# Kernel optimization log

Hardware: AMD Instinct MI355X
Metric: run time of the kernel (lower is better)

Reference implementation:

```python
import jax, jax.numpy as jnp
import numpy as np

N = 50000      # nodes
E = 1600000    # edges
R = 12         # relations (num_unique_edge_attrs)
F_IN = 64      # num_node_features
H = 128        # hidden_channels
C = 10         # num_classes
G = 256        # graphs in batch
EPS = 1e-5     # BatchNorm eps


def setup_inputs() -> dict:
    key = jax.random.key(0)
    ks = jax.random.split(key, 10)
    s = 0.05
    return {
        "x": jax.random.normal(ks[0], (N, F_IN), jnp.float32),
        "Wrel1": jax.random.normal(ks[1], (R, F_IN, H), jnp.float32) * s,
        "root1": jax.random.normal(ks[2], (F_IN, H), jnp.float32) * s,
        "bias1": jnp.zeros((H,), jnp.float32),
        "gamma1": jnp.ones((H,), jnp.float32),
        "beta1": jnp.zeros((H,), jnp.float32),
        "Wrel2": jax.random.normal(ks[3], (R, H, H), jnp.float32) * s,
        "root2": jax.random.normal(ks[4], (H, H), jnp.float32) * s,
        "bias2": jnp.zeros((H,), jnp.float32),
        "gamma2": jnp.ones((H,), jnp.float32),
        "beta2": jnp.zeros((H,), jnp.float32),
        "Wf": jax.random.normal(ks[5], (H, C), jnp.float32) * s,
        "bf": jnp.zeros((C,), jnp.float32),
        "edge_index": jax.random.randint(ks[6], (2, E), 0, N, dtype=jnp.int64) if jax.config.jax_enable_x64 else jax.random.randint(ks[6], (2, E), 0, N),
        "edge_type": jax.random.randint(ks[7], (E,), 0, R),
        "batch": jnp.sort(jax.random.randint(ks[8], (N,), 0, G)),
    }


def _segment_mean(vals, idx, num):
    # mean aggregation; empty segments -> 0
    s = jax.ops.segment_sum(vals, idx, num_segments=num)
    c = jax.ops.segment_sum(jnp.ones(idx.shape, vals.dtype), idx, num_segments=num)
    return s / jnp.clip(c, 1.0)[:, None]


def _rgcn(x, Wrel, root, bias, src, dst, edge_type):
    # PyG RGCNConv with aggr='mean': per-relation mean of source features, then W_r
    seg = dst * R + edge_type                      # fused (node, relation) segment id
    h = _segment_mean(x[src], seg, N * R)          # [N*R, in]
    h = h.reshape(N, R, x.shape[1])
    return jnp.einsum('nri,rio->no', h, Wrel) + x @ root + bias


def _bn(x, gamma, beta):
    # BatchNorm1d training-mode math (batch statistics, biased variance)
    mu = jnp.mean(x, axis=0)
    var = jnp.mean((x - mu) ** 2, axis=0)
    return gamma * (x - mu) / jnp.sqrt(var + EPS) + beta


def reference(x, Wrel1, root1, bias1, gamma1, beta1,
              Wrel2, root2, bias2, gamma2, beta2,
              Wf, bf, edge_index, edge_type, batch):
    src, dst = edge_index[0], edge_index[1]
    h = jax.nn.relu(_bn(_rgcn(x, Wrel1, root1, bias1, src, dst, edge_type), gamma1, beta1))
    h = jax.nn.relu(_bn(_rgcn(h, Wrel2, root2, bias2, src, dst, edge_type), gamma2, beta2))
    pooled = _segment_mean(h, batch, G)            # global_mean_pool -> [G, H]
    return pooled @ Wf + bf                        # [G, C]
```

## Files before the change

kernel.cpp:

```cpp
#include <hip/hip_runtime.h>

constexpr int N_NODES = 50000;
constexpr int N_EDGES = 1600000;
constexpr int NREL    = 12;
constexpr int F_INPUT = 64;
constexpr int HID     = 128;
constexpr int NCLS    = 10;
constexpr int NGRAPH  = 256;
constexpr float BN_EPS = 1e-5f;

constexpr int NB    = 391;
constexpr int SEGB  = 128 * NREL;
constexpr int NOFF  = NB * SEGB;
constexpr int NBB   = NB * 2;
constexpr int NBLK  = 392;
constexpr int PTPB  = 1024;
constexpr int EPB   = 4096;

typedef float v4f __attribute__((ext_vector_type(4)));
typedef short s8b __attribute__((ext_vector_type(8)));

__device__ __forceinline__ unsigned f2bf(float f) {
    unsigned u = __float_as_uint(f);
    return (u + 0x7FFFu + ((u >> 16) & 1u)) >> 16;
}
__device__ __forceinline__ unsigned pack2(float a, float b) {
    return f2bf(a) | (f2bf(b) << 16);
}
__device__ __forceinline__ float bflo(unsigned u) { return __uint_as_float(u << 16); }
__device__ __forceinline__ float bfhi(unsigned u) { return __uint_as_float(u & 0xFFFF0000u); }

constexpr int PQ0 = 64;
constexpr int PQ1 = PQ0 + 64;
constexpr int PQ2 = PQ1 + 8192;
constexpr int PQ3 = PQ2 + 13 * F_INPUT * HID;
constexpr int PQ4 = PQ3 + 13 * HID * HID;
constexpr int PQ5 = PQ4 + N_NODES * F_INPUT / 4;
constexpr int PQ6 = PQ5 + NGRAPH;
constexpr int PREP_BLOCKS = (PQ6 + 255) / 256;

__global__ void prep(const float* __restrict__ Wrel1, const float* __restrict__ root1,
                     const float* __restrict__ Wrel2, const float* __restrict__ root2,
                     const float* __restrict__ x, const int* __restrict__ batch,
                     ushort* __restrict__ Wp1, ushort* __restrict__ Wp2,
                     ushort* __restrict__ xb,
                     float* __restrict__ bn1, float* __restrict__ bn2,
                     float* __restrict__ psum, float* __restrict__ pcnt) {
    int tid = blockIdx.x * 256 + threadIdx.x;
    const uint4 z = make_uint4(0, 0, 0, 0);
    if (tid < PQ0) { reinterpret_cast<uint4*>(bn1)[tid] = z; return; }
    if (tid < PQ1) { reinterpret_cast<uint4*>(bn2)[tid - PQ0] = z; return; }
    if (tid < PQ2) { reinterpret_cast<uint4*>(psum)[tid - PQ1] = z; return; }
    if (tid < PQ3) {
        int idx = tid - PQ2;
        int r = idx >> 13, rem = idx & 8191;
        int k = rem >> 7, n = rem & 127;
        const float* W = (r < NREL) ? (Wrel1 + (size_t)r * 8192) : root1;
        float v = W[k * HID + n];
        int b = k >> 5, kk = k & 31;
        int j = (n & 7) * 16 + (n >> 3);
        Wp1[(((size_t)(r * 2 + b)) * HID + j) * 32 + kk] = (ushort)f2bf(v);
        return;
    }
    if (tid < PQ4) {
        int idx = tid - PQ3;
        int r = idx >> 14, rem = idx & 16383;
        int k = rem >> 7, n = rem & 127;
        const float* W = (r < NREL) ? (Wrel2 + (size_t)r * 16384) : root2;
        float v = W[k * HID + n];
        int b = k >> 5, kk = k & 31;
        int j = (n & 7) * 16 + (n >> 3);
        Wp2[(((size_t)(r * 4 + b)) * HID + j) * 32 + kk] = (ushort)f2bf(v);
        return;
    }
    if (tid < PQ5) {
        int i = tid - PQ4;
        float4 v = reinterpret_cast<const float4*>(x)[i];
        uint2 o;
        o.x = pack2(v.x, v.y);
        o.y = pack2(v.z, v.w);
        reinterpret_cast<uint2*>(xb)[i] = o;
        return;
    }
    if (tid < PQ6) {
        int g = tid - PQ5;
        int lo0 = 0, hi0 = N_NODES;
        while (lo0 < hi0) { int m = (lo0 + hi0) >> 1; if (batch[m] < g) lo0 = m + 1; else hi0 = m; }
        int lo1 = lo0, hi1 = N_NODES;
        while (lo1 < hi1) { int m = (lo1 + hi1) >> 1; if (batch[m] < g + 1) lo1 = m + 1; else hi1 = m; }
        pcnt[g] = (float)(lo1 - lo0);
    }
}


__global__ __launch_bounds__(PTPB)
void part_hist(const int* __restrict__ dst, int* __restrict__ histG) {
    __shared__ int h[NB];
    int t = threadIdx.x, blk = blockIdx.x;
    if (t < NB) h[t] = 0;
    __syncthreads();
    int base = blk * EPB;
#pragma unroll
    for (int it = 0; it < EPB / PTPB; ++it) {
        int e = base + it * PTPB + t;
        if (e < N_EDGES) atomicAdd(&h[dst[e] >> 7], 1);
    }
    __syncthreads();
    if (t < NB) histG[blk * NB + t] = h[t];
}

__global__ __launch_bounds__(512)
void part_scanA(const int* __restrict__ histG, int* __restrict__ cursorG,
                int* __restrict__ bucketTot) {
    __shared__ int s[512];
    int t = threadIdx.x, b = blockIdx.x;
    int v = (t < NBLK) ? histG[t * NB + b] : 0;
    s[t] = v;
    __syncthreads();
    for (int d = 1; d < 512; d <<= 1) {
        int x = (t >= d) ? s[t - d] : 0;
        __syncthreads();
        s[t] += x;
        __syncthreads();
    }
    if (t < NBLK) cursorG[t * NB + b] = s[t] - v;
    if (t == NBLK - 1) bucketTot[b] = s[t];
}

__global__ __launch_bounds__(512)
void part_scanB(const int* __restrict__ bucketTot, int* __restrict__ bucketBase) {
    __shared__ int s[512];
    int t = threadIdx.x;
    int v = (t < NB) ? bucketTot[t] : 0;
    s[t] = v;
    __syncthreads();
    for (int d = 1; d < 512; d <<= 1) {
        int x = (t >= d) ? s[t - d] : 0;
        __syncthreads();
        s[t] += x;
        __syncthreads();
    }
    if (t <= NB) bucketBase[t] = (t == 0) ? 0 : s[t - 1];
}

__global__ __launch_bounds__(PTPB)
void part_scatter(const int* __restrict__ src, const int* __restrict__ dst,
                  const int* __restrict__ et, const int* __restrict__ cursorG,
                  const int* __restrict__ bucketBase, uint* __restrict__ ebuck) {
    __shared__ int cur[NB];
    int t = threadIdx.x, blk = blockIdx.x;
    if (t < NB) cur[t] = cursorG[blk * NB + t] + bucketBase[t];
    __syncthreads();
    int base = blk * EPB;
#pragma unroll
    for (int it = 0; it < EPB / PTPB; ++it) {
        int e = base + it * PTPB + t;
        if (e < N_EDGES) {
            int d = dst[e];
            int b = d >> 7;
            int pos = atomicAdd(&cur[b], 1);
            ebuck[pos] = (uint)src[e] | ((uint)(d & 127) << 16) | ((uint)et[e] << 23);
        }
    }
}

__global__ __launch_bounds__(256)
void csr_finalize(const uint* __restrict__ ebuck, const int* __restrict__ bucketBase,
                  int* __restrict__ off, uint* __restrict__ zpack) {
    __shared__ int cnt[SEGB];
    __shared__ int cur[SEGB];
    __shared__ int partial[256];
    int t = threadIdx.x, b = blockIdx.x;
    int eb0 = bucketBase[b], eb1 = bucketBase[b + 1];
#pragma unroll
    for (int i = 0; i < 6; ++i) cnt[t * 6 + i] = 0;
    __syncthreads();
    for (int e = eb0 + t; e < eb1; e += 256) {
        uint u = ebuck[e];
        int key = (int)(u >> 23) * 128 + (int)((u >> 16) & 127);
        atomicAdd(&cnt[key], 1);
    }
    __syncthreads();
    int loc[6];
    int sum = 0;
#pragma unroll
    for (int i = 0; i < 6; ++i) { loc[i] = sum; sum += cnt[t * 6 + i]; }
    partial[t] = sum;
    __syncthreads();
    for (int d = 1; d < 256; d <<= 1) {
        int v = (t >= d) ? partial[t - d] : 0;
        __syncthreads();
        partial[t] += v;
        __syncthreads();
    }
    int tbase = (t == 0) ? 0 : partial[t - 1];
#pragma unroll
    for (int i = 0; i < 6; ++i) {
        int s = t * 6 + i;
        int gpos = eb0 + tbase + loc[i];
        cur[s] = gpos;
        off[b * SEGB + s] = gpos;
    }
    __syncthreads();
    for (int e = eb0 + t; e < eb1; e += 256) {
        uint u = ebuck[e];
        int key = (int)(u >> 23) * 128 + (int)((u >> 16) & 127);
        int pos = atomicAdd(&cur[key], 1);
        zpack[pos] = u & 0x7FFFFFu;
    }
    if (b == 0 && t == 0) off[NOFF] = N_EDGES;
}


template <int F>
__global__ __launch_bounds__(256)
void gemm_fused(const ushort* __restrict__ X, const int* __restrict__ offR,
                const uint* __restrict__ zpack, const ushort* __restrict__ Wp,
                const float* __restrict__ bias, float* __restrict__ H,
                float* __restrict__ bn_sum, float* __restrict__ bn_sq) {
    constexpr int FP2 = F + 8;
    constexpr int KB  = F / 32;
    constexpr int CH  = 8;
    __shared__ __align__(16) ushort A[4][2][16 * FP2];
    __shared__ float BNred[2][4][HID];
    const int t = threadIdx.x;
    const int lane = t & 63, wave = t >> 6, q = lane >> 4, l16 = lane & 15;
    const int bid = blockIdx.x;
    const int bucket = bid >> 1, h = bid & 1;
    const int rowbase = h * 64 + wave * 16;
    const int n0 = bucket * 128 + rowbase;
    const int obase = bucket * SEGB + rowbase;

    ushort* Aw0 = A[wave][0];
    ushort* Aw1 = A[wave][1];

    auto zerorow = [&](ushort* Ab, int r) {
        if constexpr (F == 64) Ab[r * FP2 + lane] = 0;
        else *reinterpret_cast<uint*>(Ab + r * FP2 + lane * 2) = 0u;
    };

    float a0, a1;
    auto build = [&](int rel, ushort* Ab) {
        if (rel == NREL) {
#pragma unroll 4
            for (int i = 0; i < 16; ++i) {
                int n = n0 + i;
                if constexpr (F == 64) {
                    Ab[i * FP2 + lane] = (n < N_NODES) ? X[(size_t)n * 64 + lane] : (ushort)0;
                } else {
                    uint v = (n < N_NODES)
                        ? *reinterpret_cast<const uint*>(X + (size_t)n * 128 + lane * 2) : 0u;
                    *reinterpret_cast<uint*>(Ab + i * FP2 + lane * 2) = v;
                }
            }
            return;
        }
        const int i0 = obase + rel * 128;
        const int e0 = offR[i0];
        const int e1 = offR[i0 + 16];
        if (e0 >= e1) {
            for (int r = 0; r < 16; ++r) zerorow(Ab, r);
            return;
        }
        a0 = 0.f; a1 = 0.f;
        int ln = 0, eStart = e0;
        auto flush = [&](int r, int cntE) {
            float winv = (cntE > 0) ? 1.f / (float)cntE : 0.f;
            if constexpr (F == 64)
                Ab[r * FP2 + lane] = (ushort)f2bf(a0 * winv);
            else
                *reinterpret_cast<uint*>(Ab + r * FP2 + lane * 2) = pack2(a0 * winv, a1 * winv);
            a0 = 0.f; a1 = 0.f;
        };
        const int elast = e1 - 1;
        auto ldpk = [&](int e, uint* p) {
#pragma unroll
            for (int j = 0; j < CH; ++j) p[j] = zpack[min(e + j, elast)];
        };
        auto ldux = [&](const uint* p, uint* u) {
#pragma unroll
            for (int j = 0; j < CH; ++j) {
                int s = (int)(p[j] & 0xFFFFu);
                if constexpr (F == 64)
                    u[j] = X[(size_t)s * 64 + lane];
                else
                    u[j] = *reinterpret_cast<const uint*>(X + (size_t)s * 128 + lane * 2);
            }
        };
        uint pk[CH], ux[CH];
        ldpk(e0, pk);
        ldux(pk, ux);
        for (int e = e0; e < e1; e += CH) {
            uint pn[CH], un[CH];
            if (e + CH < e1) { ldpk(e + CH, pn); ldux(pn, un); }
#pragma unroll
            for (int j = 0; j < CH; ++j) {
                int ej = e + j;
                if (ej < e1) {
                    int ld = (int)(pk[j] >> 16) - rowbase;
                    if (ld != ln) {
                        flush(ln, ej - eStart);
                        for (int z = ln + 1; z < ld; ++z) zerorow(Ab, z);
                        ln = ld; eStart = ej;
                    }
                    a0 += bflo(ux[j]);
                    if constexpr (F == 128) a1 += bfhi(ux[j]);
                }
            }
#pragma unroll
            for (int j = 0; j < CH; ++j) { pk[j] = pn[j]; ux[j] = un[j]; }
        }
        flush(ln, e1 - eStart);
        for (int z = ln + 1; z < 16; ++z) zerorow(Ab, z);
    };

    v4f acc[8];
#pragma unroll
    for (int nt = 0; nt < 8; ++nt) acc[nt] = (v4f){0.f, 0.f, 0.f, 0.f};

    build(0, Aw0);
    for (int rel = 0; rel <= NREL; ++rel) {
        ushort* Acur = (rel & 1) ? Aw1 : Aw0;
        ushort* Anxt = (rel & 1) ? Aw0 : Aw1;
        if (rel < NREL) build(rel + 1, Anxt);
#pragma unroll
        for (int kb = 0; kb < KB; ++kb) {
            s8b bfr[8];
            const ushort* wb = Wp + ((size_t)(rel * KB + kb) * HID + l16) * 32 + q * 8;
#pragma unroll
            for (int nt = 0; nt < 8; ++nt)
                bfr[nt] = *reinterpret_cast<const s8b*>(wb + (size_t)nt * 16 * 32);
            s8b af = *reinterpret_cast<const s8b*>(Acur + l16 * FP2 + kb * 32 + q * 8);
#pragma unroll
            for (int nt = 0; nt < 8; ++nt)
                acc[nt] = __builtin_amdgcn_mfma_f32_16x16x32_bf16(af, bfr[nt], acc[nt], 0, 0, 0);
        }
    }

    const int c0 = l16 * 8;
    float4 b4a = *reinterpret_cast<const float4*>(bias + c0);
    float4 b4b = *reinterpret_cast<const float4*>(bias + c0 + 4);
    float bv[8] = {b4a.x, b4a.y, b4a.z, b4a.w, b4b.x, b4b.y, b4b.z, b4b.w};
    float s[8], sq[8];
#pragma unroll
    for (int nt = 0; nt < 8; ++nt) { s[nt] = 0.f; sq[nt] = 0.f; }
#pragma unroll
    for (int rr = 0; rr < 4; ++rr) {
        int n = n0 + q * 4 + rr;
        if (n < N_NODES) {
            float v[8];
#pragma unroll
            for (int nt = 0; nt < 8; ++nt) {
                v[nt] = acc[nt][rr] + bv[nt];
                s[nt] += v[nt];
                sq[nt] += v[nt] * v[nt];
            }
            float* hr = H + (size_t)n * HID + c0;
            *reinterpret_cast<float4*>(hr)     = make_float4(v[0], v[1], v[2], v[3]);
            *reinterpret_cast<float4*>(hr + 4) = make_float4(v[4], v[5], v[6], v[7]);
        }
    }
#pragma unroll
    for (int nt = 0; nt < 8; ++nt) {
        s[nt]  += __shfl_xor(s[nt], 16);  s[nt]  += __shfl_xor(s[nt], 32);
        sq[nt] += __shfl_xor(sq[nt], 16); sq[nt] += __shfl_xor(sq[nt], 32);
    }
    if (q == 0) {
#pragma unroll
        for (int nt = 0; nt < 8; ++nt) {
            BNred[0][wave][c0 + nt] = s[nt];
            BNred[1][wave][c0 + nt] = sq[nt];
        }
    }
    __syncthreads();
    if (t < HID) {
        atomicAdd(&bn_sum[t], BNred[0][0][t] + BNred[0][1][t] + BNred[0][2][t] + BNred[0][3][t]);
    } else {
        int c = t - HID;
        atomicAdd(&bn_sq[c], BNred[1][0][c] + BNred[1][1][c] + BNred[1][2][c] + BNred[1][3][c]);
    }
}


__global__ void bn_relu_bf16(const float* __restrict__ h, const float* __restrict__ bn_sum,
                             const float* __restrict__ bn_sq, const float* __restrict__ gamma,
                             const float* __restrict__ beta, ushort* __restrict__ outb) {
    __shared__ float CA[HID], CB[HID];
    int t = threadIdx.x;
    if (t < HID) {
        float mu = bn_sum[t] * (1.0f / N_NODES);
        float var = bn_sq[t] * (1.0f / N_NODES) - mu * mu;
        float a = gamma[t] / sqrtf(var + BN_EPS);
        CA[t] = a;
        CB[t] = beta[t] - a * mu;
    }
    __syncthreads();
    int i = blockIdx.x * 256 + t;
    constexpr int TOTAL = N_NODES * HID / 4;
    if (i < TOTAL) {
        int o4 = i & 31;
        float4 a = reinterpret_cast<const float4*>(CA)[o4];
        float4 b = reinterpret_cast<const float4*>(CB)[o4];
        float4 v = reinterpret_cast<const float4*>(h)[i];
        v.x = fmaxf(a.x * v.x + b.x, 0.f);
        v.y = fmaxf(a.y * v.y + b.y, 0.f);
        v.z = fmaxf(a.z * v.z + b.z, 0.f);
        v.w = fmaxf(a.w * v.w + b.w, 0.f);
        uint2 o;
        o.x = pack2(v.x, v.y);
        o.y = pack2(v.z, v.w);
        reinterpret_cast<uint2*>(outb)[i] = o;
    }
}


__global__ void pool_bnrelu(const float* __restrict__ h, const float* __restrict__ bn_sum,
                            const float* __restrict__ bn_sq, const float* __restrict__ gamma,
                            const float* __restrict__ beta, const int* __restrict__ batch,
                            float* __restrict__ psum) {
    __shared__ float CA[HID], CB[HID];
    int t = threadIdx.x;
    if (t < HID) {
        float mu = bn_sum[t] * (1.0f / N_NODES);
        float var = bn_sq[t] * (1.0f / N_NODES) - mu * mu;
        float a = gamma[t] / sqrtf(var + BN_EPS);
        CA[t] = a;
        CB[t] = beta[t] - a * mu;
    }
    __syncthreads();
    int col = t & 127;
    int nb = blockIdx.x * 16 + (t >> 7) * 8;
    float a = CA[col], b = CB[col];
    float run = 0.f;
    int curg = -1;
    for (int i = 0; i < 8; ++i) {
        int n = nb + i;
        if (n < N_NODES) {
            int g = batch[n];
            float v = fmaxf(a * h[(size_t)n * HID + col] + b, 0.f);
            if (g != curg) {
                if (curg >= 0) atomicAdd(&psum[curg * HID + col], run);
                run = 0.f;
                curg = g;
            }
            run += v;
        }
    }
    if (curg >= 0) atomicAdd(&psum[curg * HID + col], run);
}

__global__ void final_kernel(const float* __restrict__ psum, const float* __restrict__ pcnt,
                             const float* __restrict__ Wf, const float* __restrict__ bf,
                             float* __restrict__ out) {
    __shared__ float p[HID];
    int g = blockIdx.x, t = threadIdx.x;
    float inv = 1.0f / fmaxf(pcnt[g], 1.0f);
    p[t] = psum[g * HID + t] * inv;
    p[t + 64] = psum[g * HID + t + 64] * inv;
    __syncthreads();
    if (t < NCLS) {
        float s = bf[t];
#pragma unroll 16
        for (int k = 0; k < HID; ++k) s += p[k] * Wf[k * NCLS + t];
        out[g * NCLS + t] = s;
    }
}


extern "C" void kernel_launch(void* const* d_in, const int* in_sizes, int n_in,
                              void* d_out, int out_size, void* d_ws, size_t ws_size,
                              hipStream_t stream) {
    const float* x      = (const float*)d_in[0];
    const float* Wrel1  = (const float*)d_in[1];
    const float* root1  = (const float*)d_in[2];
    const float* bias1  = (const float*)d_in[3];
    const float* gamma1 = (const float*)d_in[4];
    const float* beta1  = (const float*)d_in[5];
    const float* Wrel2  = (const float*)d_in[6];
    const float* root2  = (const float*)d_in[7];
    const float* bias2  = (const float*)d_in[8];
    const float* gamma2 = (const float*)d_in[9];
    const float* beta2  = (const float*)d_in[10];
    const float* Wf     = (const float*)d_in[11];
    const float* bf     = (const float*)d_in[12];
    const int* ei       = (const int*)d_in[13];
    const int* et       = (const int*)d_in[14];
    const int* batch    = (const int*)d_in[15];
    const int* srcv = ei;
    const int* dstv = ei + N_EDGES;

    char* w = (char*)d_ws;
    auto alloc = [&](size_t bytes) -> char* {
        char* p = w;
        w += (bytes + 255) / 256 * 256;
        return p;
    };
    int* off     = (int*)alloc((size_t)(NOFF + 1) * 4);
    uint* zpack  = (uint*)alloc((size_t)N_EDGES * 4);
    ushort* xb   = (ushort*)alloc((size_t)N_NODES * F_INPUT * 2);
    ushort* H1b  = (ushort*)alloc((size_t)N_NODES * HID * 2);
    ushort* Wp1  = (ushort*)alloc((size_t)13 * F_INPUT * HID * 2);
    ushort* Wp2  = (ushort*)alloc((size_t)13 * HID * HID * 2);
    float* bn1   = (float*)alloc(2 * HID * 4);
    float* bn2   = (float*)alloc(2 * HID * 4);
    float* psum  = (float*)alloc((size_t)NGRAPH * HID * 4);
    float* pcnt  = (float*)alloc((size_t)NGRAPH * 4);
    float* Hbuf  = (float*)alloc((size_t)N_NODES * HID * 4);
    int* histG      = (int*)alloc((size_t)NBLK * NB * 4);
    int* cursorG    = (int*)alloc((size_t)NBLK * NB * 4);
    int* bucketTot  = (int*)alloc((size_t)NB * 4);
    int* bucketBase = (int*)alloc((size_t)(NB + 1) * 4);
    uint* ebuck     = (uint*)alloc((size_t)N_EDGES * 4);

    prep<<<PREP_BLOCKS, 256, 0, stream>>>(Wrel1, root1, Wrel2, root2, x, batch,
                                          Wp1, Wp2, xb, bn1, bn2, psum, pcnt);

    part_hist<<<NBLK, PTPB, 0, stream>>>(dstv, histG);
    part_scanA<<<NB, 512, 0, stream>>>(histG, cursorG, bucketTot);
    part_scanB<<<1, 512, 0, stream>>>(bucketTot, bucketBase);
    part_scatter<<<NBLK, PTPB, 0, stream>>>(srcv, dstv, et, cursorG, bucketBase, ebuck);
    csr_finalize<<<NB, 256, 0, stream>>>(ebuck, bucketBase, off, zpack);

    gemm_fused<F_INPUT><<<NBB, 256, 0, stream>>>(xb, off, zpack, Wp1, bias1,
                                                 Hbuf, bn1, bn1 + HID);
    bn_relu_bf16<<<(N_NODES * HID / 4 + 255) / 256, 256, 0, stream>>>(Hbuf, bn1, bn1 + HID,
                                                                      gamma1, beta1, H1b);

    gemm_fused<HID><<<NBB, 256, 0, stream>>>(H1b, off, zpack, Wp2, bias2,
                                             Hbuf, bn2, bn2 + HID);

    pool_bnrelu<<<(N_NODES + 15) / 16, 256, 0, stream>>>(Hbuf, bn2, bn2 + HID, gamma2, beta2,
                                                         batch, psum);
    final_kernel<<<NGRAPH, 64, 0, stream>>>(psum, pcnt, Wf, bf, (float*)d_out);
}
```

Before: 485.9 us.

## Split relation loop across two blocks with atomic output and separate BN stats kernel

Each 64-row tile of the fused RGCN gather+GEMM now runs as two blocks, one for relations 0-5 and one for relations 6-12 including root. Both blocks accumulate into a zeroed output buffer with float atomics, which doubles the grid to raise parallelism on the gather-bound phase. The in-kernel double-buffered A tile is dropped for a deeper three-stage register prefetch of edges. Because the partial results are combined by atomics, BatchNorm statistics move to a new grid-stride reduction kernel. This costs extra passes over the output buffer, zero-initialisation of two large buffers, and nondeterministic float atomic ordering.

```diff
diff --git a/kernel.cpp b/kernel.cpp
--- a/kernel.cpp
+++ b/kernel.cpp
@@ -37,7 +37,9 @@
 constexpr int PQ4 = PQ3 + 13 * HID * HID;
 constexpr int PQ5 = PQ4 + N_NODES * F_INPUT / 4;
 constexpr int PQ6 = PQ5 + NGRAPH;
-constexpr int PREP_BLOCKS = (PQ6 + 255) / 256;
+constexpr int PQ7 = PQ6 + N_NODES * HID / 4;
+constexpr int PQ8 = PQ7 + N_NODES * HID / 4;
+constexpr int PREP_BLOCKS = (PQ8 + 255) / 256;
 
 __global__ void prep(const float* __restrict__ Wrel1, const float* __restrict__ root1,
                      const float* __restrict__ Wrel2, const float* __restrict__ root2,
@@ -45,7 +47,8 @@
                      ushort* __restrict__ Wp1, ushort* __restrict__ Wp2,
                      ushort* __restrict__ xb,
                      float* __restrict__ bn1, float* __restrict__ bn2,
-                     float* __restrict__ psum, float* __restrict__ pcnt) {
+                     float* __restrict__ psum, float* __restrict__ pcnt,
+                     float* __restrict__ h1, float* __restrict__ h2) {
     int tid = blockIdx.x * 256 + threadIdx.x;
     const uint4 z = make_uint4(0, 0, 0, 0);
     if (tid < PQ0) { reinterpret_cast<uint4*>(bn1)[tid] = z; return; }
@@ -89,7 +92,10 @@
         int lo1 = lo0, hi1 = N_NODES;
         while (lo1 < hi1) { int m = (lo1 + hi1) >> 1; if (batch[m] < g + 1) lo1 = m + 1; else hi1 = m; }
         pcnt[g] = (float)(lo1 - lo0);
-    }
+        return;
+    }
+    if (tid < PQ7) { reinterpret_cast<uint4*>(h1)[tid - PQ6] = z; return; }
+    if (tid < PQ8) { reinterpret_cast<uint4*>(h2)[tid - PQ7] = z; return; }
 }
 
 
@@ -216,31 +222,102 @@
 __global__ __launch_bounds__(256)
 void gemm_fused(const ushort* __restrict__ X, const int* __restrict__ offR,
                 const uint* __restrict__ zpack, const ushort* __restrict__ Wp,
-                const float* __restrict__ bias, float* __restrict__ H,
-                float* __restrict__ bn_sum, float* __restrict__ bn_sq) {
+                const float* __restrict__ bias, float* __restrict__ H) {
     constexpr int FP2 = F + 8;
     constexpr int KB  = F / 32;
     constexpr int CH  = 8;
-    __shared__ __align__(16) ushort A[4][2][16 * FP2];
-    __shared__ float BNred[2][4][HID];
+    __shared__ __align__(16) ushort A[4][16 * FP2];
     const int t = threadIdx.x;
     const int lane = t & 63, wave = t >> 6, q = lane >> 4, l16 = lane & 15;
     const int bid = blockIdx.x;
-    const int bucket = bid >> 1, h = bid & 1;
+    const int split = bid & 1;
+    const int hb = bid >> 1;
+    const int bucket = hb >> 1, h = hb & 1;
     const int rowbase = h * 64 + wave * 16;
     const int n0 = bucket * 128 + rowbase;
     const int obase = bucket * SEGB + rowbase;
-
-    ushort* Aw0 = A[wave][0];
-    ushort* Aw1 = A[wave][1];
-
-    auto zerorow = [&](ushort* Ab, int r) {
+    ushort* Ab = A[wave];
+
+    auto zerorow = [&](int r) {
         if constexpr (F == 64) Ab[r * FP2 + lane] = 0;
         else *reinterpret_cast<uint*>(Ab + r * FP2 + lane * 2) = 0u;
     };
 
-    float a0, a1;
-    auto build = [&](int rel, ushort* Ab) {
+    auto buildrel = [&](int rel) -> bool {
+        const int i0 = obase + rel * 128;
+        const int e0 = offR[i0];
+        const int e1 = offR[i0 + 16];
+        if (e0 >= e1) return false;
+        const int elast = e1 - 1;
+        float a0 = 0.f, a1 = 0.f;
+        int ln = 0, eStart = e0;
+        auto flush = [&](int r, int cntE) {
+            float winv = (cntE > 0) ? 1.f / (float)cntE : 0.f;
+            if constexpr (F == 64)
+                Ab[r * FP2 + lane] = (ushort)f2bf(a0 * winv);
+            else
+                *reinterpret_cast<uint*>(Ab + r * FP2 + lane * 2) = pack2(a0 * winv, a1 * winv);
+            a0 = 0.f; a1 = 0.f;
+        };
+        auto ldpk = [&](int e, uint* p) {
+#pragma unroll
+            for (int j = 0; j < CH; ++j) p[j] = zpack[min(e + j, elast)];
+        };
+        auto ldux = [&](const uint* p, uint* u) {
+#pragma unroll
+            for (int j = 0; j < CH; ++j) {
+                int s = (int)(p[j] & 0xFFFFu);
+                if constexpr (F == 64)
+                    u[j] = X[(size_t)s * 64 + lane];
+                else
+                    u[j] = *reinterpret_cast<const uint*>(X + (size_t)s * 128 + lane * 2);
+            }
+        };
+        uint pk0[CH], pk1[CH], pk2[CH], ux0[CH], ux1[CH];
+        ldpk(e0, pk0);
+        ldux(pk0, ux0);
+        ldpk(e0 + CH, pk1);
+        ldux(pk1, ux1);
+        ldpk(e0 + 2 * CH, pk2);
+        const int nch = (e1 - e0 + CH - 1) / CH;
+        for (int c = 0; c < nch; ++c) {
+            uint ux2[CH], pk3[CH];
+            ldux(pk2, ux2);
+            ldpk(e0 + (c + 3) * CH, pk3);
+            const int ebase = e0 + c * CH;
+#pragma unroll
+            for (int j = 0; j < CH; ++j) {
+                int ej = ebase + j;
+                if (ej < e1) {
+                    int ld = (int)(pk0[j] >> 16) - rowbase;
+                    if (ld != ln) {
+                        flush(ln, ej - eStart);
+                        for (int z = ln + 1; z < ld; ++z) zerorow(z);
+                        ln = ld; eStart = ej;
+                    }
+                    a0 += bflo(ux0[j]);
+                    if constexpr (F == 128) a1 += bfhi(ux0[j]);
+                }
+            }
+#pragma unroll
+            for (int j = 0; j < CH; ++j) {
+                pk0[j] = pk1[j]; pk1[j] = pk2[j]; pk2[j] = pk3[j];
+                ux0[j] = ux1[j]; ux1[j] = ux2[j];
+            }
+        }
+        flush(ln, e1 - eStart);
+        for (int z = ln + 1; z < 16; ++z) zerorow(z);
+        return true;
+    };
+
+    v4f acc[8];
+#pragma unroll
+    for (int nt = 0; nt < 8; ++nt) acc[nt] = (v4f){0.f, 0.f, 0.f, 0.f};
+
+    const int r0 = split ? 6 : 0;
+    const int r1 = split ? 13 : 6;
+    for (int rel = r0; rel < r1; ++rel) {
+        bool have;
         if (rel == NREL) {
 #pragma unroll 4
             for (int i = 0; i < 16; ++i) {
@@ -253,132 +330,73 @@
                     *reinterpret_cast<uint*>(Ab + i * FP2 + lane * 2) = v;
                 }
             }
-            return;
+            have = true;
+        } else {
+            have = buildrel(rel);
         }
-        const int i0 = obase + rel * 128;
-        const int e0 = offR[i0];
-        const int e1 = offR[i0 + 16];
-        if (e0 >= e1) {
-            for (int r = 0; r < 16; ++r) zerorow(Ab, r);
-            return;
+        if (have) {
+#pragma unroll
+            for (int kb = 0; kb < KB; ++kb) {
+                s8b bfr[8];
+                const ushort* wb = Wp + ((size_t)(rel * KB + kb) * HID + l16) * 32 + q * 8;
+#pragma unroll
+                for (int nt = 0; nt < 8; ++nt)
+                    bfr[nt] = *reinterpret_cast<const s8b*>(wb + (size_t)nt * 16 * 32);
+                s8b af = *reinterpret_cast<const s8b*>(Ab + l16 * FP2 + kb * 32 + q * 8);
+#pragma unroll
+                for (int nt = 0; nt < 8; ++nt)
+                    acc[nt] = __builtin_amdgcn_mfma_f32_16x16x32_bf16(af, bfr[nt], acc[nt], 0, 0, 0);
+            }
         }
-        a0 = 0.f; a1 = 0.f;
-        int ln = 0, eStart = e0;
-        auto flush = [&](int r, int cntE) {
-            float winv = (cntE > 0) ? 1.f / (float)cntE : 0.f;
-            if constexpr (F == 64)
-                Ab[r * FP2 + lane] = (ushort)f2bf(a0 * winv);
-            else
-                *reinterpret_cast<uint*>(Ab + r * FP2 + lane * 2) = pack2(a0 * winv, a1 * winv);
-            a0 = 0.f; a1 = 0.f;
-        };
-        const int elast = e1 - 1;
-        auto ldpk = [&](int e, uint* p) {
-#pragma unroll
-            for (int j = 0; j < CH; ++j) p[j] = zpack[min(e + j, elast)];
-        };
-        auto ldux = [&](const uint* p, uint* u) {
-#pragma unroll
-            for (int j = 0; j < CH; ++j) {
-                int s = (int)(p[j] & 0xFFFFu);
-                if constexpr (F == 64)
-                    u[j] = X[(size_t)s * 64 + lane];
-                else
-                    u[j] = *reinterpret_cast<const uint*>(X + (size_t)s * 128 + lane * 2);
-            }
-        };
-        uint pk[CH], ux[CH];
-        ldpk(e0, pk);
-        ldux(pk, ux);
-        for (int e = e0; e < e1; e += CH) {
-            uint pn[CH], un[CH];
-            if (e + CH < e1) { ldpk(e + CH, pn); ldux(pn, un); }
-#pragma unroll
-            for (int j = 0; j < CH; ++j) {
-                int ej = e + j;
-                if (ej < e1) {
-                    int ld = (int)(pk[j] >> 16) - rowbase;
-                    if (ld != ln) {
-                        flush(ln, ej - eStart);
-                        for (int z = ln + 1; z < ld; ++z) zerorow(Ab, z);
-                        ln = ld; eStart = ej;
-                    }
-                    a0 += bflo(ux[j]);
-                    if constexpr (F == 128) a1 += bfhi(ux[j]);
-                }
-            }
-#pragma unroll
-            for (int j = 0; j < CH; ++j) { pk[j] = pn[j]; ux[j] = un[j]; }
-        }
-        flush(ln, e1 - eStart);
-        for (int z = ln + 1; z < 16; ++z) zerorow(Ab, z);
-    };
-
-    v4f acc[8];
-#pragma unroll
-    for (int nt = 0; nt < 8; ++nt) acc[nt] = (v4f){0.f, 0.f, 0.f, 0.f};
-
-    build(0, Aw0);
-    for (int rel = 0; rel <= NREL; ++rel) {
-        ushort* Acur = (rel & 1) ? Aw1 : Aw0;
-        ushort* Anxt = (rel & 1) ? Aw0 : Aw1;
-        if (rel < NREL) build(rel + 1, Anxt);
-#pragma unroll
-        for (int kb = 0; kb < KB; ++kb) {
-            s8b bfr[8];
-            const ushort* wb = Wp + ((size_t)(rel * KB + kb) * HID + l16) * 32 + q * 8;
-#pragma unroll
-            for (int nt = 0; nt < 8; ++nt)
-                bfr[nt] = *reinterpret_cast<const s8b*>(wb + (size_t)nt * 16 * 32);
-            s8b af = *reinterpret_cast<const s8b*>(Acur + l16 * FP2 + kb * 32 + q * 8);
-#pragma unroll
-            for (int nt = 0; nt < 8; ++nt)
-                acc[nt] = __builtin_amdgcn_mfma_f32_16x16x32_bf16(af, bfr[nt], acc[nt], 0, 0, 0);
-        }
     }
 
     const int c0 = l16 * 8;
-    float4 b4a = *reinterpret_cast<const float4*>(bias + c0);
-    float4 b4b = *reinterpret_cast<const float4*>(bias + c0 + 4);
-    float bv[8] = {b4a.x, b4a.y, b4a.z, b4a.w, b4b.x, b4b.y, b4b.z, b4b.w};
-    float s[8], sq[8];
-#pragma unroll
-    for (int nt = 0; nt < 8; ++nt) { s[nt] = 0.f; sq[nt] = 0.f; }
+    float bv[8];
+    if (split) {
+        float4 b4a = *reinterpret_cast<const float4*>(bias + c0);
+        float4 b4b = *reinterpret_cast<const float4*>(bias + c0 + 4);
+        bv[0] = b4a.x; bv[1] = b4a.y; bv[2] = b4a.z; bv[3] = b4a.w;
+        bv[4] = b4b.x; bv[5] = b4b.y; bv[6] = b4b.z; bv[7] = b4b.w;
+    } else {
+#pragma unroll
+        for (int k = 0; k < 8; ++k) bv[k] = 0.f;
+    }
 #pragma unroll
     for (int rr = 0; rr < 4; ++rr) {
         int n = n0 + q * 4 + rr;
         if (n < N_NODES) {
-            float v[8];
-#pragma unroll
-            for (int nt = 0; nt < 8; ++nt) {
-                v[nt] = acc[nt][rr] + bv[nt];
-                s[nt] += v[nt];
-                sq[nt] += v[nt] * v[nt];
-            }
             float* hr = H + (size_t)n * HID + c0;
-            *reinterpret_cast<float4*>(hr)     = make_float4(v[0], v[1], v[2], v[3]);
-            *reinterpret_cast<float4*>(hr + 4) = make_float4(v[4], v[5], v[6], v[7]);
+#pragma unroll
+            for (int nt = 0; nt < 8; ++nt)
+                atomicAdd(&hr[nt], acc[nt][rr] + bv[nt]);
         }
     }
-#pragma unroll
-    for (int nt = 0; nt < 8; ++nt) {
-        s[nt]  += __shfl_xor(s[nt], 16);  s[nt]  += __shfl_xor(s[nt], 32);
-        sq[nt] += __shfl_xor(sq[nt], 16); sq[nt] += __shfl_xor(sq[nt], 32);
-    }
-    if (q == 0) {
-#pragma unroll
-        for (int nt = 0; nt < 8; ++nt) {
-            BNred[0][wave][c0 + nt] = s[nt];
-            BNred[1][wave][c0 + nt] = sq[nt];
-        }
-    }
-    __syncthreads();
-    if (t < HID) {
-        atomicAdd(&bn_sum[t], BNred[0][0][t] + BNred[0][1][t] + BNred[0][2][t] + BNred[0][3][t]);
-    } else {
-        int c = t - HID;
-        atomicAdd(&bn_sq[c], BNred[1][0][c] + BNred[1][1][c] + BNred[1][2][c] + BNred[1][3][c]);
-    }
+}
+
+
+constexpr int BNS_BLOCKS = 512;
+__global__ __launch_bounds__(256)
+void bn_stats(const float* __restrict__ H, float* __restrict__ bn) {
+    __shared__ float red[2 * HID];
+    int t = threadIdx.x;
+    red[t] = 0.f;
+    __syncthreads();
+    float s[4] = {0.f, 0.f, 0.f, 0.f}, sq[4] = {0.f, 0.f, 0.f, 0.f};
+    constexpr int TOT4 = N_NODES * HID / 4;
+    const int stride = BNS_BLOCKS * 256;
+    for (int i = blockIdx.x * 256 + t; i < TOT4; i += stride) {
+        float4 v = reinterpret_cast<const float4*>(H)[i];
+        s[0] += v.x; s[1] += v.y; s[2] += v.z; s[3] += v.w;
+        sq[0] += v.x * v.x; sq[1] += v.y * v.y; sq[2] += v.z * v.z; sq[3] += v.w * v.w;
+    }
+    int c4 = (t & 31) * 4;
+#pragma unroll
+    for (int k = 0; k < 4; ++k) {
+        atomicAdd(&red[c4 + k], s[k]);
+        atomicAdd(&red[HID + c4 + k], sq[k]);
+    }
+    __syncthreads();
+    atomicAdd(&bn[t], red[t]);
 }
 
 
@@ -505,7 +523,8 @@
     float* bn2   = (float*)alloc(2 * HID * 4);
     float* psum  = (float*)alloc((size_t)NGRAPH * HID * 4);
     float* pcnt  = (float*)alloc((size_t)NGRAPH * 4);
-    float* Hbuf  = (float*)alloc((size_t)N_NODES * HID * 4);
+    float* Hbuf1 = (float*)alloc((size_t)N_NODES * HID * 4);
+    float* Hbuf2 = (float*)alloc((size_t)N_NODES * HID * 4);
     int* histG      = (int*)alloc((size_t)NBLK * NB * 4);
     int* cursorG    = (int*)alloc((size_t)NBLK * NB * 4);
     int* bucketTot  = (int*)alloc((size_t)NB * 4);
@@ -513,7 +532,8 @@
     uint* ebuck     = (uint*)alloc((size_t)N_EDGES * 4);
 
     prep<<<PREP_BLOCKS, 256, 0, stream>>>(Wrel1, root1, Wrel2, root2, x, batch,
-                                          Wp1, Wp2, xb, bn1, bn2, psum, pcnt);
+                                          Wp1, Wp2, xb, bn1, bn2, psum, pcnt,
+                                          Hbuf1, Hbuf2);
 
     part_hist<<<NBLK, PTPB, 0, stream>>>(dstv, histG);
     part_scanA<<<NB, 512, 0, stream>>>(histG, cursorG, bucketTot);
@@ -521,15 +541,15 @@
     part_scatter<<<NBLK, PTPB, 0, stream>>>(srcv, dstv, et, cursorG, bucketBase, ebuck);
     csr_finalize<<<NB, 256, 0, stream>>>(ebuck, bucketBase, off, zpack);
 
-    gemm_fused<F_INPUT><<<NBB, 256, 0, stream>>>(xb, off, zpack, Wp1, bias1,
-                                                 Hbuf, bn1, bn1 + HID);
-    bn_relu_bf16<<<(N_NODES * HID / 4 + 255) / 256, 256, 0, stream>>>(Hbuf, bn1, bn1 + HID,
+    gemm_fused<F_INPUT><<<NBB * 2, 256, 0, stream>>>(xb, off, zpack, Wp1, bias1, Hbuf1);
+    bn_stats<<<BNS_BLOCKS, 256, 0, stream>>>(Hbuf1, bn1);
+    bn_relu_bf16<<<(N_NODES * HID / 4 + 255) / 256, 256, 0, stream>>>(Hbuf1, bn1, bn1 + HID,
                                                                       gamma1, beta1, H1b);
 
-    gemm_fused<HID><<<NBB, 256, 0, stream>>>(H1b, off, zpack, Wp2, bias2,
-                                             Hbuf, bn2, bn2 + HID);
-
-    pool_bnrelu<<<(N_NODES + 15) / 16, 256, 0, stream>>>(Hbuf, bn2, bn2 + HID, gamma2, beta2,
+    gemm_fused<HID><<<NBB * 2, 256, 0, stream>>>(H1b, off, zpack, Wp2, bias2, Hbuf2);
+    bn_stats<<<BNS_BLOCKS, 256, 0, stream>>>(Hbuf2, bn2);
+
+    pool_bnrelu<<<(N_NODES + 15) / 16, 256, 0, stream>>>(Hbuf2, bn2, bn2 + HID, gamma2, beta2,
                                                          batch, psum);
     final_kernel<<<NGRAPH, 64, 0, stream>>>(psum, pcnt, Wf, bf, (float*)d_out);
 }
```

New measurement: 1.178 ms. 2.42x slower.
